# Optimization experiments

Measured on AMD Instinct MI355X. Metric: run time of the kernel, lower is better.

The kernel has to match this reference:

```python
import jax, jax.numpy as jnp
import numpy as np
import math

B, S, HID, H = 1, 512, 256, 8
D = HID // H
SCALE = 1.0 / math.sqrt(D)
PI = math.pi


def setup_inputs() -> dict:
    key = jax.random.key(0)
    ks = jax.random.split(key, 6)
    x = jax.random.normal(ks[0], (B, S, HID), dtype=jnp.float32)
    w = lambda k: jax.random.normal(k, (HID, HID), dtype=jnp.float32) * 0.02
    return {
        'x': x,
        'wq': w(ks[1]), 'bq': jnp.zeros((HID,), jnp.float32),
        'wk': w(ks[2]), 'bk': jnp.zeros((HID,), jnp.float32),
        'wv': w(ks[3]), 'bv': jnp.zeros((HID,), jnp.float32),
        'wo': w(ks[4]), 'bo': jnp.zeros((HID,), jnp.float32),
    }


def _split_heads(t):
    # [B,S,HID] -> [B,H,S,D]
    return t.reshape(B, S, H, D).transpose(0, 2, 1, 3)


def reference(x, wq, bq, wk, bk, wv, bv, wo, bo):
    # Linear projections (torch nn.Linear: x @ W.T + b)
    q = _split_heads(x @ wq.T + bq)
    k = _split_heads(x @ wk.T + bk)
    v = _split_heads(x @ wv.T + bv)

    omega = jax.nn.sigmoid(q) * PI      # [B,H,S,D]
    amplitude = jax.nn.sigmoid(k)       # [B,H,S,D]
    phase = jnp.tanh(v) * PI            # [B,H,S,D]

    # relative position i-j, [S,S]
    pos = (jnp.arange(S)[:, None] - jnp.arange(S)[None, :]).astype(jnp.float32)
    # wave interference tensor [B,H,S,D,S] (query i, dim d, key j)
    interaction = amplitude[..., None] * jnp.cos(
        omega[..., None] * pos[None, None, :, None, :] + phase[..., None])
    patterns = jax.nn.softmax(interaction * SCALE, axis=-1)  # softmax over keys j
    # contract over key positions: per-dim attention
    context = jnp.einsum('bhidj,bhjd->bhid', patterns, v)    # [B,H,S,D]
    context = context.transpose(0, 2, 1, 3).reshape(B, S, HID)
    return context @ wo.T + bo
```

## Files before the change

kernel.cpp:

```cpp
#include <hip/hip_runtime.h>
#include <math.h>

#define SEQ 512
#define HID 256
#define NH 8
#define DH 32
#define PI_F 3.14159265358979323846f
#define SCALE_F 0.17677669529663687f
#define LOG2E_F 1.4426950408889634f

#define OFF_OMEGA 0
#define OFF_AMP   131072
#define OFF_PHASE 262144
#define OFF_V     393216
#define OFF_CTX   524288

__device__ __forceinline__ float sigmoidf_(float x) { return 1.f / (1.f + expf(-x)); }

__global__ __launch_bounds__(256) void gemm_fused(
    const float* __restrict__ A,
    const float* __restrict__ W0, const float* __restrict__ W1,
    const float* __restrict__ W2,
    const float* __restrict__ bq, const float* __restrict__ bk,
    const float* __restrict__ bv, const float* __restrict__ bo,
    float* __restrict__ ws, float* __restrict__ outp, int mode_base)
{
    const int mode = mode_base + blockIdx.y;
    const float* W    = (mode == 1) ? W1 : (mode == 2) ? W2 : W0;
    const float* bias = (mode == 0) ? bq : (mode == 1) ? bk : (mode == 2) ? bv : bo;

    const int bx = blockIdx.x;
    const int ct = bx & 3;
    const int rt = bx >> 2;
    const int r0 = rt * 32, c0 = ct * 64;

    __shared__ float xs[32 * 68];
    __shared__ float wts[64 * 64];

    const int tid = threadIdx.x;
    const int rg = tid >> 4, cg = tid & 15;

    float acc[2][4];
#pragma unroll
    for (int i = 0; i < 2; i++)
#pragma unroll
        for (int j = 0; j < 4; j++) acc[i][j] = 0.f;

    for (int kc = 0; kc < 4; kc++) {
        const int k0 = kc * 64;
#pragma unroll
        for (int it = 0; it < 4; it++) {
            int idx = tid + it * 256;
            int rr = idx >> 4, f4 = idx & 15;
            float4 wv = *(const float4*)(W + (c0 + rr) * HID + k0 + 4 * f4);
            int cw = rr ^ ((f4 & 7) << 2);
            wts[(4 * f4 + 0) * 64 + cw] = wv.x;
            wts[(4 * f4 + 1) * 64 + cw] = wv.y;
            wts[(4 * f4 + 2) * 64 + cw] = wv.z;
            wts[(4 * f4 + 3) * 64 + cw] = wv.w;
            if (it < 2) {
                float4 av = *(const float4*)(A + (r0 + rr) * HID + k0 + 4 * f4);
                *(float4*)&xs[rr * 68 + 4 * f4] = av;
            }
        }
        __syncthreads();

#pragma unroll
        for (int g = 0; g < 16; g++) {
            float xfa[2][4], wfa[4][4];
#pragma unroll
            for (int i = 0; i < 2; i++) {
                float4 xv = *(const float4*)&xs[(2 * rg + i) * 68 + 4 * g];
                xfa[i][0] = xv.x; xfa[i][1] = xv.y; xfa[i][2] = xv.z; xfa[i][3] = xv.w;
            }
            const int sw = (g & 7) << 2;
#pragma unroll
            for (int m = 0; m < 4; m++) {
                float4 wv = *(const float4*)&wts[(4 * g + m) * 64 + ((4 * cg) ^ sw)];
                wfa[m][0] = wv.x; wfa[m][1] = wv.y; wfa[m][2] = wv.z; wfa[m][3] = wv.w;
            }
#pragma unroll
            for (int m = 0; m < 4; m++)
#pragma unroll
                for (int i = 0; i < 2; i++)
#pragma unroll
                    for (int j = 0; j < 4; j++)
                        acc[i][j] = fmaf(xfa[i][m], wfa[m][j], acc[i][j]);
        }
        __syncthreads();
    }

    float4 b4 = *(const float4*)&bias[c0 + 4 * cg];
#pragma unroll
    for (int i = 0; i < 2; i++) {
        const int r = r0 + 2 * rg + i;
        const int o = r * HID + c0 + 4 * cg;
        float s0 = acc[i][0] + b4.x;
        float s1 = acc[i][1] + b4.y;
        float s2 = acc[i][2] + b4.z;
        float s3 = acc[i][3] + b4.w;
        if (mode == 0) {
            float4 t;
            t.x = PI_F * sigmoidf_(s0); t.y = PI_F * sigmoidf_(s1);
            t.z = PI_F * sigmoidf_(s2); t.w = PI_F * sigmoidf_(s3);
            *(float4*)&ws[OFF_OMEGA + o] = t;
        } else if (mode == 1) {
            float4 t;
            t.x = sigmoidf_(s0); t.y = sigmoidf_(s1);
            t.z = sigmoidf_(s2); t.w = sigmoidf_(s3);
            *(float4*)&ws[OFF_AMP + o] = t;
        } else if (mode == 2) {
            float4 t; t.x = s0; t.y = s1; t.z = s2; t.w = s3;
            *(float4*)&ws[OFF_V + o] = t;
            float4 p;
            p.x = PI_F * tanhf(s0); p.y = PI_F * tanhf(s1);
            p.z = PI_F * tanhf(s2); p.w = PI_F * tanhf(s3);
            *(float4*)&ws[OFF_PHASE + o] = p;
        } else {
            float4 t; t.x = s0; t.y = s1; t.z = s2; t.w = s3;
            *(float4*)&outp[o] = t;
        }
    }
}

__global__ __launch_bounds__(256) void wave_attn(const float* __restrict__ ws,
                                                 float* __restrict__ ctx)
{
    const int h  = blockIdx.y;
    const int il = threadIdx.x >> 5;
    const int d  = threadIdx.x & 31;
    const int i  = blockIdx.x * 8 + il;
    const int col = h * DH + d;

    const float w  = ws[OFF_OMEGA + i * HID + col];
    const float aL = ws[OFF_AMP + i * HID + col] * (SCALE_F * LOG2E_F);
    const float ph = ws[OFF_PHASE + i * HID + col];
    const float* vcol = ws + OFF_V + col;

    float sw_, cw;
    sincosf(w, &sw_, &cw);
    float c2 = cw * cw - sw_ * sw_, s2 = 2.f * sw_ * cw;
    float c4 = c2 * c2 - s2 * s2;

    float th0 = fmaf(w, (float)i, ph);
    float c_, s_;
    sincosf(th0, &s_, &c_);

    float pPrev[4], pCur[4];
#pragma unroll
    for (int k = 0; k < 4; k++) {
        pPrev[k] = aL * c_;
        float nc = c_ * cw + s_ * sw_;
        float ns = s_ * cw - c_ * sw_;
        c_ = nc; s_ = ns;
    }
#pragma unroll
    for (int k = 0; k < 4; k++) {
        pCur[k] = aL * c_;
        float nc = c_ * cw + s_ * sw_;
        float ns = s_ * cw - c_ * sw_;
        c_ = nc; s_ = ns;
    }
    const float C2 = 2.f * c4;

    float den[4], num[4];
#pragma unroll
    for (int k = 0; k < 4; k++) { den[k] = 0.f; num[k] = 0.f; }

#pragma unroll 4
    for (int t = 0; t < SEQ / 4; t++) {
        float v0 = vcol[(4 * t + 0) * HID];
        float v1 = vcol[(4 * t + 1) * HID];
        float v2v = vcol[(4 * t + 2) * HID];
        float v3 = vcol[(4 * t + 3) * HID];
        float e0 = __builtin_amdgcn_exp2f(pPrev[0]);
        float e1 = __builtin_amdgcn_exp2f(pPrev[1]);
        float e2 = __builtin_amdgcn_exp2f(pPrev[2]);
        float e3 = __builtin_amdgcn_exp2f(pPrev[3]);
        den[0] += e0; den[1] += e1; den[2] += e2; den[3] += e3;
        num[0] = fmaf(e0, v0, num[0]);
        num[1] = fmaf(e1, v1, num[1]);
        num[2] = fmaf(e2, v2v, num[2]);
        num[3] = fmaf(e3, v3, num[3]);
#pragma unroll
        for (int k = 0; k < 4; k++) {
            float nx = fmaf(C2, pCur[k], -pPrev[k]);
            pPrev[k] = pCur[k]; pCur[k] = nx;
        }
    }
    float denom = (den[0] + den[1]) + (den[2] + den[3]);
    float numer = (num[0] + num[1]) + (num[2] + num[3]);
    ctx[i * HID + col] = numer / denom;
}

extern "C" void kernel_launch(void* const* d_in, const int* in_sizes, int n_in,
                              void* d_out, int out_size, void* d_ws, size_t ws_size,
                              hipStream_t stream) {
    const float* x  = (const float*)d_in[0];
    const float* wq = (const float*)d_in[1];
    const float* bq = (const float*)d_in[2];
    const float* wk = (const float*)d_in[3];
    const float* bk = (const float*)d_in[4];
    const float* wv = (const float*)d_in[5];
    const float* bv = (const float*)d_in[6];
    const float* wo = (const float*)d_in[7];
    const float* bo = (const float*)d_in[8];

    float* ws = (float*)d_ws;

    hipLaunchKernelGGL(gemm_fused, dim3(64, 3), dim3(256), 0, stream,
                       x, wq, wk, wv, bq, bk, bv, bo, ws, (float*)d_out, 0);
    hipLaunchKernelGGL(wave_attn, dim3(SEQ / 8, NH), dim3(256), 0, stream,
                       ws, ws + OFF_CTX);
    hipLaunchKernelGGL(gemm_fused, dim3(64, 1), dim3(256), 0, stream,
                       ws + OFF_CTX, wo, wo, wo, bq, bk, bv, bo, ws,
                       (float*)d_out, 3);
}
```

Measured before the change: 99.95 us.

## Fuse projection, wave attention and output GEMM into one cooperative kernel

```diff
diff --git a/kernel.cpp b/kernel.cpp
--- a/kernel.cpp
+++ b/kernel.cpp
@@ -1,4 +1,5 @@
 #include <hip/hip_runtime.h>
+#include <hip/hip_cooperative_groups.h>
 #include <math.h>
 
 #define SEQ 512
@@ -17,28 +18,16 @@
 
 __device__ __forceinline__ float sigmoidf_(float x) { return 1.f / (1.f + expf(-x)); }
 
-__global__ __launch_bounds__(256) void gemm_fused(
-    const float* __restrict__ A,
-    const float* __restrict__ W0, const float* __restrict__ W1,
-    const float* __restrict__ W2,
-    const float* __restrict__ bq, const float* __restrict__ bk,
-    const float* __restrict__ bv, const float* __restrict__ bo,
-    float* __restrict__ ws, float* __restrict__ outp, int mode_base)
+__device__ __forceinline__ void gemm_tile(
+    const float* __restrict__ A, const float* __restrict__ W,
+    const float* __restrict__ bias, float* __restrict__ ws,
+    float* __restrict__ outp, int mode, int bx, int tid,
+    float* xs, float* wts)
 {
-    const int mode = mode_base + blockIdx.y;
-    const float* W    = (mode == 1) ? W1 : (mode == 2) ? W2 : W0;
-    const float* bias = (mode == 0) ? bq : (mode == 1) ? bk : (mode == 2) ? bv : bo;
-
-    const int bx = blockIdx.x;
     const int ct = bx & 3;
     const int rt = bx >> 2;
     const int r0 = rt * 32, c0 = ct * 64;
-
-    __shared__ float xs[32 * 68];
-    __shared__ float wts[64 * 64];
-
-    const int tid = threadIdx.x;
-    const int rg = tid >> 4, cg = tid & 15;
+    const int rg = tid >> 4, cgi = tid & 15;
 
     float acc[2][4];
 #pragma unroll
@@ -76,7 +65,7 @@
             const int sw = (g & 7) << 2;
 #pragma unroll
             for (int m = 0; m < 4; m++) {
-                float4 wv = *(const float4*)&wts[(4 * g + m) * 64 + ((4 * cg) ^ sw)];
+                float4 wv = *(const float4*)&wts[(4 * g + m) * 64 + ((4 * cgi) ^ sw)];
                 wfa[m][0] = wv.x; wfa[m][1] = wv.y; wfa[m][2] = wv.z; wfa[m][3] = wv.w;
             }
 #pragma unroll
@@ -90,11 +79,11 @@
         __syncthreads();
     }
 
-    float4 b4 = *(const float4*)&bias[c0 + 4 * cg];
+    float4 b4 = *(const float4*)&bias[c0 + 4 * cgi];
 #pragma unroll
     for (int i = 0; i < 2; i++) {
         const int r = r0 + 2 * rg + i;
-        const int o = r * HID + c0 + 4 * cg;
+        const int o = r * HID + c0 + 4 * cgi;
         float s0 = acc[i][0] + b4.x;
         float s1 = acc[i][1] + b4.y;
         float s2 = acc[i][2] + b4.z;
@@ -123,74 +112,100 @@
     }
 }
 
-__global__ __launch_bounds__(256) void wave_attn(const float* __restrict__ ws,
-                                                 float* __restrict__ ctx)
+__global__ __launch_bounds__(256) void fused_all(
+    const float* __restrict__ x,
+    const float* __restrict__ wq, const float* __restrict__ wk,
+    const float* __restrict__ wv, const float* __restrict__ wo,
+    const float* __restrict__ bq, const float* __restrict__ bk,
+    const float* __restrict__ bv, const float* __restrict__ bo,
+    float* __restrict__ ws, float* __restrict__ out)
 {
-    const int h  = blockIdx.y;
-    const int il = threadIdx.x >> 5;
-    const int d  = threadIdx.x & 31;
-    const int i  = blockIdx.x * 8 + il;
-    const int col = h * DH + d;
-
-    const float w  = ws[OFF_OMEGA + i * HID + col];
-    const float aL = ws[OFF_AMP + i * HID + col] * (SCALE_F * LOG2E_F);
-    const float ph = ws[OFF_PHASE + i * HID + col];
-    const float* vcol = ws + OFF_V + col;
-
-    float sw_, cw;
-    sincosf(w, &sw_, &cw);
-    float c2 = cw * cw - sw_ * sw_, s2 = 2.f * sw_ * cw;
-    float c4 = c2 * c2 - s2 * s2;
-
-    float th0 = fmaf(w, (float)i, ph);
-    float c_, s_;
-    sincosf(th0, &s_, &c_);
-
-    float pPrev[4], pCur[4];
-#pragma unroll
-    for (int k = 0; k < 4; k++) {
-        pPrev[k] = aL * c_;
-        float nc = c_ * cw + s_ * sw_;
-        float ns = s_ * cw - c_ * sw_;
-        c_ = nc; s_ = ns;
-    }
-#pragma unroll
-    for (int k = 0; k < 4; k++) {
-        pCur[k] = aL * c_;
-        float nc = c_ * cw + s_ * sw_;
-        float ns = s_ * cw - c_ * sw_;
-        c_ = nc; s_ = ns;
-    }
-    const float C2 = 2.f * c4;
-
-    float den[4], num[4];
-#pragma unroll
-    for (int k = 0; k < 4; k++) { den[k] = 0.f; num[k] = 0.f; }
+    __shared__ float xs[32 * 68];
+    __shared__ float wts[64 * 64];
+    const int bid = blockIdx.x;
+    const int tid = threadIdx.x;
+
+    if (bid < 192) {
+        const int mode = bid >> 6;
+        const int bx = bid & 63;
+        const float* W    = (mode == 1) ? wk : (mode == 2) ? wv : wq;
+        const float* bias = (mode == 0) ? bq : (mode == 1) ? bk : bv;
+        gemm_tile(x, W, bias, ws, out, mode, bx, tid, xs, wts);
+    }
+    cooperative_groups::this_grid().sync();
+
+    {
+        const int h  = bid >> 6;
+        const int il = tid >> 5;
+        const int d  = tid & 31;
+        const int i  = (bid & 63) * 8 + il;
+        const int col = h * DH + d;
+
+        const float w  = ws[OFF_OMEGA + i * HID + col];
+        const float aL = ws[OFF_AMP + i * HID + col] * (SCALE_F * LOG2E_F);
+        const float ph = ws[OFF_PHASE + i * HID + col];
+        const float* vcol = ws + OFF_V + col;
+
+        float sw_, cw;
+        sincosf(w, &sw_, &cw);
+        float c2 = cw * cw - sw_ * sw_, s2 = 2.f * sw_ * cw;
+        float c4 = c2 * c2 - s2 * s2;
+
+        float th0 = fmaf(w, (float)i, ph);
+        float c_, s_;
+        sincosf(th0, &s_, &c_);
+
+        float pPrev[4], pCur[4];
+#pragma unroll
+        for (int k = 0; k < 4; k++) {
+            pPrev[k] = aL * c_;
+            float nc = c_ * cw + s_ * sw_;
+            float ns = s_ * cw - c_ * sw_;
+            c_ = nc; s_ = ns;
+        }
+#pragma unroll
+        for (int k = 0; k < 4; k++) {
+            pCur[k] = aL * c_;
+            float nc = c_ * cw + s_ * sw_;
+            float ns = s_ * cw - c_ * sw_;
+            c_ = nc; s_ = ns;
+        }
+        const float C2 = 2.f * c4;
+
+        float den[4], num[4];
+#pragma unroll
+        for (int k = 0; k < 4; k++) { den[k] = 0.f; num[k] = 0.f; }
 
 #pragma unroll 4
-    for (int t = 0; t < SEQ / 4; t++) {
-        float v0 = vcol[(4 * t + 0) * HID];
-        float v1 = vcol[(4 * t + 1) * HID];
-        float v2v = vcol[(4 * t + 2) * HID];
-        float v3 = vcol[(4 * t + 3) * HID];
-        float e0 = __builtin_amdgcn_exp2f(pPrev[0]);
-        float e1 = __builtin_amdgcn_exp2f(pPrev[1]);
-        float e2 = __builtin_amdgcn_exp2f(pPrev[2]);
-        float e3 = __builtin_amdgcn_exp2f(pPrev[3]);
-        den[0] += e0; den[1] += e1; den[2] += e2; den[3] += e3;
-        num[0] = fmaf(e0, v0, num[0]);
-        num[1] = fmaf(e1, v1, num[1]);
-        num[2] = fmaf(e2, v2v, num[2]);
-        num[3] = fmaf(e3, v3, num[3]);
-#pragma unroll
-        for (int k = 0; k < 4; k++) {
-            float nx = fmaf(C2, pCur[k], -pPrev[k]);
-            pPrev[k] = pCur[k]; pCur[k] = nx;
-        }
-    }
-    float denom = (den[0] + den[1]) + (den[2] + den[3]);
-    float numer = (num[0] + num[1]) + (num[2] + num[3]);
-    ctx[i * HID + col] = numer / denom;
+        for (int t = 0; t < SEQ / 4; t++) {
+            float v0 = vcol[(4 * t + 0) * HID];
+            float v1 = vcol[(4 * t + 1) * HID];
+            float v2v = vcol[(4 * t + 2) * HID];
+            float v3 = vcol[(4 * t + 3) * HID];
+            float e0 = __builtin_amdgcn_exp2f(pPrev[0]);
+            float e1 = __builtin_amdgcn_exp2f(pPrev[1]);
+            float e2 = __builtin_amdgcn_exp2f(pPrev[2]);
+            float e3 = __builtin_amdgcn_exp2f(pPrev[3]);
+            den[0] += e0; den[1] += e1; den[2] += e2; den[3] += e3;
+            num[0] = fmaf(e0, v0, num[0]);
+            num[1] = fmaf(e1, v1, num[1]);
+            num[2] = fmaf(e2, v2v, num[2]);
+            num[3] = fmaf(e3, v3, num[3]);
+#pragma unroll
+            for (int k = 0; k < 4; k++) {
+                float nx = fmaf(C2, pCur[k], -pPrev[k]);
+                pPrev[k] = pCur[k]; pCur[k] = nx;
+            }
+        }
+        float denom = (den[0] + den[1]) + (den[2] + den[3]);
+        float numer = (num[0] + num[1]) + (num[2] + num[3]);
+        ws[OFF_CTX + i * HID + col] = numer / denom;
+    }
+    cooperative_groups::this_grid().sync();
+
+    if (bid < 64) {
+        gemm_tile(ws + OFF_CTX, wo, bo, ws, out, 3, bid, tid, xs, wts);
+    }
 }
 
 extern "C" void kernel_launch(void* const* d_in, const int* in_sizes, int n_in,
@@ -206,13 +221,11 @@
     const float* wo = (const float*)d_in[7];
     const float* bo = (const float*)d_in[8];
 
-    float* ws = (float*)d_ws;
-
-    hipLaunchKernelGGL(gemm_fused, dim3(64, 3), dim3(256), 0, stream,
-                       x, wq, wk, wv, bq, bk, bv, bo, ws, (float*)d_out, 0);
-    hipLaunchKernelGGL(wave_attn, dim3(SEQ / 8, NH), dim3(256), 0, stream,
-                       ws, ws + OFF_CTX);
-    hipLaunchKernelGGL(gemm_fused, dim3(64, 1), dim3(256), 0, stream,
-                       ws + OFF_CTX, wo, wo, wo, bq, bk, bv, bo, ws,
-                       (float*)d_out, 3);
+    float* wsp  = (float*)d_ws;
+    float* outp = (float*)d_out;
+
+    void* args[] = {(void*)&x,  (void*)&wq, (void*)&wk, (void*)&wv, (void*)&wo,
+                    (void*)&bq, (void*)&bk, (void*)&bv, (void*)&bo,
+                    (void*)&wsp, (void*)&outp};
+    hipLaunchCooperativeKernel(fused_all, dim3(512), dim3(256), args, 0, stream);
 }
```

After: 234.3 us. 134% more time.
